# Kernel tuning notes

Measured on AMD Instinct MI355X. Metric: run time of the kernel, lower is better.

## Reference

```python
import jax, jax.numpy as jnp
import numpy as np

B, DIM, OC, H, W, HEADS = 4, 128, 128, 128, 128, 8
L = H * W
_BN_INV = 1.0 / (1.0 + 1e-5) ** 0.5  # eval-mode BN: running_mean=0, running_var=1


def conv2d(x, w, b=None, groups=1, pad=0):
    y = jax.lax.conv_general_dilated(
        x, w, (1, 1), [(pad, pad), (pad, pad)],
        dimension_numbers=('NCHW', 'OIHW', 'NCHW'),
        feature_group_count=groups)
    if b is not None:
        y = y + b[None, :, None, None]
    return y


def bn(x, g, b):
    return x * (g * _BN_INV)[None, :, None, None] + b[None, :, None, None]


def ln(x, g, b, eps=1e-5):
    m = jnp.mean(x, -1, keepdims=True)
    v = jnp.mean((x - m) ** 2, -1, keepdims=True)
    return (x - m) * jax.lax.rsqrt(v + eps) * g + b


def rope_tables(h, w, c, base=10000.0):
    k_max = c // 4
    theta = 1.0 / base ** (np.arange(k_max, dtype=np.float32) / k_max)
    gi, gj = np.meshgrid(np.arange(h, dtype=np.float32),
                         np.arange(w, dtype=np.float32), indexing='ij')
    ang = np.concatenate([gi[..., None] * theta, gj[..., None] * theta], -1)  # (h,w,c//2)
    return jnp.asarray(np.cos(ang)), jnp.asarray(np.sin(ang))


def apply_rope(x, cs, sn):  # x: (b,h,w,c); consecutive pairs = (re, im)
    xr, xi = x[..., 0::2], x[..., 1::2]
    return jnp.stack([cs * xr - sn * xi, sn * xr + cs * xi], -1).reshape(x.shape)


def linear_attn(x, qk_w, qk_b, lepe_w, lepe_b, h, w):
    b, n, c = x.shape
    hd = c // HEADS
    qk = x @ qk_w.T + qk_b
    q = jax.nn.elu(qk[..., :c]) + 1.0
    k = jax.nn.elu(qk[..., c:]) + 1.0
    cs, sn = rope_tables(h, w, c)

    def heads(t):  # (b,n,c) -> (b,HEADS,n,hd)
        return t.reshape(b, n, HEADS, hd).transpose(0, 2, 1, 3)

    q_r = heads(apply_rope(q.reshape(b, h, w, c), cs, sn).reshape(b, n, c))
    k_r = heads(apply_rope(k.reshape(b, h, w, c), cs, sn).reshape(b, n, c))
    qh, kh, vh = heads(q), heads(k), heads(x)
    k_mean = jnp.mean(kh, axis=2, keepdims=True)                      # (b,Hd,1,hd)
    z = 1.0 / (jnp.einsum('bhnd,bhmd->bhnm', qh, k_mean) + 1e-6)      # (b,Hd,n,1)
    s = n ** -0.5
    kv = jnp.einsum('bhnd,bhne->bhde', k_r * s, vh * s)               # (b,Hd,hd,hd)
    out = jnp.einsum('bhnd,bhde->bhne', q_r, kv) * z
    out = out.transpose(0, 2, 1, 3).reshape(b, n, c)
    v_img = x.reshape(b, h, w, c).transpose(0, 3, 1, 2)
    lepe = conv2d(v_img, lepe_w, lepe_b, groups=c, pad=1)
    return out + lepe.transpose(0, 2, 3, 1).reshape(b, n, c)


def fmt_block(xb, fw1, fb1, f_g, f_be, fw2, fb2, n_g, n_be):
    t = jnp.fft.fft2(xb)                                              # (B,C,H,W) complex
    wgt = jax.nn.relu(bn(conv2d(t.real, fw1, fb1), f_g, f_be))
    wgt = jax.nn.sigmoid(conv2d(wgt, fw2, fb2))
    f = jnp.abs(jnp.fft.ifft2(wgt * t))
    f = jax.nn.relu(bn(f, n_g, n_be))
    return f.reshape(f.shape[0], f.shape[1], -1).transpose(0, 2, 1)   # (B,L,C)


def _forward(x, c1_w, c1_b, c1_g, c1_be, cpe1_w, cpe1_b,
             fw1, fb1, f_g, f_be, fw2, fb2, nbn_g, nbn_be,
             ln1_g, ln1_b, d3w1, d3b1, d3w2, d5w1, d5b1, d5w2,
             ap_w, ap_b, ip2_w, ip2_b, dwc2_w, dwc2_b,
             qk_w, qk_b, lepe_w, lepe_b, op_w, op_b,
             cpe2_w, cpe2_b, ln2_g, ln2_b,
             ffn_w1, ffn_b1, ffn_w2, ffn_b2, po_w,
             red_w, red_b, red_g, red_be):
    Bb, C, Hh, Ww = x.shape
    Ll = Hh * Ww
    to_img = lambda t: t.reshape(Bb, Hh, Ww, C).transpose(0, 3, 1, 2)   # (B,L,C)->(B,C,H,W)
    to_seq = lambda t: t.transpose(0, 2, 3, 1).reshape(Bb, Ll, -1)       # (B,C,H,W)->(B,L,C)

    x_0 = jax.nn.relu(bn(conv2d(x, c1_w, c1_b), c1_g, c1_be))           # (B,OC,H,W)
    xt = to_seq(x + conv2d(x, cpe1_w, cpe1_b, groups=C, pad=1))
    shortcut = xt
    fmt1 = fmt_block(to_img(xt), fw1, fb1, f_g, f_be, fw2, fb2, nbn_g, nbn_be)

    x_s = ln(xt, ln1_g, ln1_b)
    xs_img = to_img(x_s)
    x_s3 = conv2d(conv2d(xs_img, d3w1, d3b1), d3w2, None, groups=C // 2, pad=1)
    x_s5 = conv2d(conv2d(xs_img, d5w1, d5b1), d5w2, None, groups=C // 2, pad=2)
    act_res = jax.nn.silu(to_seq(conv2d(xs_img, ap_w, ap_b)))

    def branch(t):  # (B,C/2,H,W) -> (B,L,C/2)
        t = conv2d(t, ip2_w, ip2_b)
        t = jax.nn.silu(conv2d(t, dwc2_w, dwc2_b, groups=C // 2, pad=1))
        return to_seq(t)

    a3 = linear_attn(branch(x_s3), qk_w, qk_b, lepe_w, lepe_b, Hh, Ww)
    a5 = linear_attn(branch(x_s5), qk_w, qk_b, lepe_w, lepe_b, Hh, Ww)
    xs = jnp.concatenate([a3, a5], -1)
    xs = to_seq(conv2d(to_img(xs * act_res), op_w, op_b))

    xt = shortcut + xs + fmt1
    xt = xt + to_seq(conv2d(to_img(xt), cpe2_w, cpe2_b, groups=C, pad=1))
    fmt2 = fmt_block(to_img(xt), fw1, fb1, f_g, f_be, fw2, fb2, nbn_g, nbn_be)
    h2 = ln(xt, ln2_g, ln2_b)
    ffn = jax.nn.gelu(h2 @ ffn_w1.T + ffn_b1, approximate=False) @ ffn_w2.T + ffn_b2
    xt = xt + ffn + fmt2

    xo = conv2d(to_img(xt), po_w)                                        # (B,OC,H,W)
    cat = jnp.concatenate([x_0, xo], 1)
    return jax.nn.relu(bn(conv2d(cat, red_w, red_b), red_g, red_be)) + x_0


def setup_inputs():
    key = jax.random.key(0)
    it = iter(jax.random.split(key, 64))

    def w(shape, s=0.05):
        return jax.random.normal(next(it), shape, jnp.float32) * s

    d, oc = DIM, OC
    ones = lambda n: jnp.ones((n,), jnp.float32)
    zeros = lambda n: jnp.zeros((n,), jnp.float32)
    return {
        'x': jax.random.normal(next(it), (B, d, H, W), jnp.float32),
        'c1_w': w((oc, d, 1, 1)), 'c1_b': w((oc,), 0.01), 'c1_g': ones(oc), 'c1_be': zeros(oc),
        'cpe1_w': w((d, 1, 3, 3)), 'cpe1_b': w((d,), 0.01),
        'fw1': w((d // 16, d, 1, 1)), 'fb1': w((d // 16,), 0.01),
        'f_g': ones(d // 16), 'f_be': zeros(d // 16),
        'fw2': w((d, d // 16, 1, 1)), 'fb2': w((d,), 0.01),
        'nbn_g': ones(d), 'nbn_be': zeros(d),
        'ln1_g': ones(d), 'ln1_b': zeros(d),
        'd3w1': w((d, d, 1, 1)), 'd3b1': w((d,), 0.01), 'd3w2': w((d // 2, 2, 3, 3)),
        'd5w1': w((d, d, 1, 1)), 'd5b1': w((d,), 0.01), 'd5w2': w((d // 2, 2, 5, 5)),
        'ap_w': w((d, d, 1, 1)), 'ap_b': w((d,), 0.01),
        'ip2_w': w((d // 2, d // 2, 1, 1)), 'ip2_b': w((d // 2,), 0.01),
        'dwc2_w': w((d // 2, 1, 3, 3)), 'dwc2_b': w((d // 2,), 0.01),
        'qk_w': w((d, d // 2)), 'qk_b': w((d,), 0.01),
        'lepe_w': w((d // 2, 1, 3, 3)), 'lepe_b': w((d // 2,), 0.01),
        'op_w': w((d, d, 1, 1)), 'op_b': w((d,), 0.01),
        'cpe2_w': w((d, 1, 3, 3)), 'cpe2_b': w((d,), 0.01),
        'ln2_g': ones(d), 'ln2_b': zeros(d),
        'ffn_w1': w((4, d)), 'ffn_b1': w((4,), 0.01),
        'ffn_w2': w((d, 4)), 'ffn_b2': w((d,), 0.01),
        'po_w': w((oc, d, 1, 1)),
        'red_w': w((oc, 2 * oc, 1, 1)), 'red_b': w((oc,), 0.01),
        'red_g': ones(oc), 'red_be': zeros(oc),
    }


def reference(x, c1_w, c1_b, c1_g, c1_be, cpe1_w, cpe1_b,
              fw1, fb1, f_g, f_be, fw2, fb2, nbn_g, nbn_be,
              ln1_g, ln1_b, d3w1, d3b1, d3w2, d5w1, d5b1, d5w2,
              ap_w, ap_b, ip2_w, ip2_b, dwc2_w, dwc2_b,
              qk_w, qk_b, lepe_w, lepe_b, op_w, op_b,
              cpe2_w, cpe2_b, ln2_g, ln2_b,
              ffn_w1, ffn_b1, ffn_w2, ffn_b2, po_w,
              red_w, red_b, red_g, red_be):
    return _forward(x, c1_w, c1_b, c1_g, c1_be, cpe1_w, cpe1_b,
                    fw1, fb1, f_g, f_be, fw2, fb2, nbn_g, nbn_be,
                    ln1_g, ln1_b, d3w1, d3b1, d3w2, d5w1, d5b1, d5w2,
                    ap_w, ap_b, ip2_w, ip2_b, dwc2_w, dwc2_b,
                    qk_w, qk_b, lepe_w, lepe_b, op_w, op_b,
                    cpe2_w, cpe2_b, ln2_g, ln2_b,
                    ffn_w1, ffn_b1, ffn_w2, ffn_b2, po_w,
                    red_w, red_b, red_g, red_be)
```

## Files before the change

kernel.cpp:

```cpp
#include <hip/hip_runtime.h>
#include <math.h>

typedef unsigned short bf16_t;
typedef __attribute__((ext_vector_type(8))) short short8;
typedef __attribute__((ext_vector_type(4))) float f32x4;

#define B_ 4
#define C_ 128
#define H_ 128
#define W_ 128
#define L_ (H_*W_)
#define NS  ((size_t)B_*L_*C_)
#define NH  ((size_t)B_*L_*64)
#define NSP ((size_t)L_*C_)
#define PI_F 3.14159265358979323846f
#define BN_INV 0.9999950000374997f
#define THETA_SC 0.8304820237218406f
#define TOTW 157148
#define W16SHIFT 107548
#define WOFF_PO 107612
#define WOFF_RED 123996

#define W2_ 66
#define L2_ (128*W2_)

__device__ __forceinline__ float ldf(bf16_t v){ return __uint_as_float(((unsigned)v)<<16); }
__device__ __forceinline__ bf16_t f2b(float f){
  unsigned u = __float_as_uint(f);
  u += 0x7fffu + ((u>>16)&1u);
  return (bf16_t)(u>>16);
}

#define WGSLOT ((size_t)B_*8*L_)
#define ACCSZ 2304
#define CWSZ 157184
#define CW16SZF 78592
#define WSF (6*NS + 3*NH + WGSLOT + ACCSZ + CWSZ + CW16SZF + 16)
__device__ float g_ws[WSF];

__global__ void k_probe(const bf16_t* __restrict__ xb, int* __restrict__ flag){
  __shared__ int vote;
  if (threadIdx.x == 0) vote = 0;
  __syncthreads();
  int bad = 0;
  for (int i = threadIdx.x; i < 2048; i += 256) {
    float v = ldf(xb[2*i]);
    if (!(fabsf(v) < 1e6f)) bad = 1;
  }
  if (bad) atomicOr(&vote, 1);
  __syncthreads();
  if (threadIdx.x == 0) *flag = vote;
}

struct P47 { const void* p[47]; };
__device__ __constant__ int c_wsz[47] = {
  16384,128,128,128,1152,128,1024,8,8,8,1024,128,128,128,128,128,
  16384,128,1152,16384,128,3200,16384,128,4096,64,576,64,8192,128,
  576,64,16384,128,1152,128,128,128,512,4,512,128,16384,32768,128,128,128};

__global__ __launch_bounds__(256) void k_cvt(P47 ps, const int* __restrict__ flagp,
                                             float* __restrict__ dst){
  int g = blockIdx.x*256 + threadIdx.x;
  if (g >= TOTW) return;
  int fl = *flagp;
  int idx = 0, off = g;
  while (off >= c_wsz[idx]) { off -= c_wsz[idx]; idx++; }
  const void* s = ps.p[idx];
  dst[g] = fl ? ((const float*)s)[off] : ldf(((const bf16_t*)s)[off]);
}

__global__ __launch_bounds__(256) void k_cvt16(const float* __restrict__ src, bf16_t* __restrict__ dst){
  int g = blockIdx.x*256 + threadIdx.x;
  if (g >= TOTW) return;
  dst[g + (g >= W16SHIFT ? 4 : 0)] = f2b(src[g]);
}

__global__ __launch_bounds__(256) void k_fuse_red(const float* __restrict__ po,
    const float* __restrict__ rw, bf16_t* __restrict__ dst16){
  int g = blockIdx.x*256 + threadIdx.x;
  int o = g >> 7, in = g & 127;
  float acc = 0.f;
  for (int j = 0; j < 128; j++) acc += rw[o*256 + 128 + j] * po[j*128 + in];
  dst16[o*256 + 128 + in] = f2b(acc);
}

__global__ void k_zero(float* p, int n){
  int i = blockIdx.x*256 + threadIdx.x;
  if (i < n) p[i] = 0.f;
}

__device__ __forceinline__ void tw_fwd(int lane, float* tc, float* ts) {
  sincosf(-PI_F * (float)lane * (1.f/64.f), &ts[0], &tc[0]);
  int i = 1;
  #pragma unroll
  for (int m = 32; m >= 1; m >>= 1, i++) {
    int k = lane & (m-1);
    sincosf(-PI_F * (float)k / (float)m, &ts[i], &tc[i]);
  }
}
__device__ __forceinline__ void tw_inv(int lane, float* tc, float* ts) {
  int i = 0;
  #pragma unroll
  for (int m = 1; m <= 32; m <<= 1, i++) {
    int k = lane & (m-1);
    sincosf(PI_F * (float)k / (float)m, &ts[i], &tc[i]);
  }
  sincosf(PI_F * (float)lane * (1.f/64.f), &ts[6], &tc[6]);
}

__device__ __forceinline__ void fft128_fwd(float& lor, float& loi, float& hir, float& hii,
                                           int lane, const float* tc, const float* ts) {
  {
    float s = ts[0], c = tc[0];
    float ar = lor, ai = loi;
    float dr = ar - hir, di = ai - hii;
    lor = ar + hir; loi = ai + hii;
    hir = dr*c - di*s; hii = dr*s + di*c;
  }
  int i = 1;
  #pragma unroll
  for (int m = 32; m >= 1; m >>= 1, i++) {
    float s = ts[i], c = tc[i];
    bool up = (lane & m) != 0;
    {
      float orr = __shfl_xor(lor, m), oii = __shfl_xor(loi, m);
      float sr = lor + orr, si = loi + oii;
      float dr = orr - lor, di = oii - loi;
      float tr = dr*c - di*s, ti = dr*s + di*c;
      lor = up ? tr : sr; loi = up ? ti : si;
    }
    {
      float orr = __shfl_xor(hir, m), oii = __shfl_xor(hii, m);
      float sr = hir + orr, si = hii + oii;
      float dr = orr - hir, di = oii - hii;
      float tr = dr*c - di*s, ti = dr*s + di*c;
      hir = up ? tr : sr; hii = up ? ti : si;
    }
  }
}

__device__ __forceinline__ void fft128_inv(float& lor, float& loi, float& hir, float& hii,
                                           int lane, const float* tc, const float* ts) {
  int i = 0;
  #pragma unroll
  for (int m = 1; m <= 32; m <<= 1, i++) {
    float s = ts[i], c = tc[i];
    bool up = (lane & m) != 0;
    {
      float orr = __shfl_xor(lor, m), oii = __shfl_xor(loi, m);
      float qr = orr*c - oii*s, qi = orr*s + oii*c;
      float lo_r = lor + qr, lo_i = loi + qi;
      float mr = lor*c - loi*s, mi = lor*s + loi*c;
      float up_r = orr - mr, up_i = oii - mi;
      lor = up ? up_r : lo_r; loi = up ? up_i : lo_i;
    }
    {
      float orr = __shfl_xor(hir, m), oii = __shfl_xor(hii, m);
      float qr = orr*c - oii*s, qi = orr*s + oii*c;
      float lo_r = hir + qr, lo_i = hii + qi;
      float mr = hir*c - hii*s, mi = hir*s + hii*c;
      float up_r = orr - mr, up_i = oii - mi;
      hir = up ? up_r : lo_r; hii = up ? up_i : lo_i;
    }
  }
  {
    float s = ts[6], c = tc[6];
    float qr = hir*c - hii*s, qi = hir*s + hii*c;
    float pr = lor, pi = loi;
    lor = pr + qr; loi = pi + qi;
    hir = pr - qr; hii = pi - qi;
  }
}

__global__ __launch_bounds__(256) void k_fft_row_fwd_half(
    const float* __restrict__ in, float* __restrict__ re, float* __restrict__ im) {
  __shared__ float T[64*130];
  int tid = threadIdx.x;
  int bid = blockIdx.x;
  int ch = (bid & 1) * 64;
  int h  = (bid >> 1) & 127;
  int b  = bid >> 8;
  const float* ip = in + ((size_t)b*L_ + (size_t)h*128)*128 + ch;
  #pragma unroll
  for (int it = 0; it < 8; it++) {
    int idx = it*256 + tid;
    int c4 = (idx & 15)*4, w = idx >> 4;
    float4 v = *(const float4*)(ip + (size_t)w*128 + c4);
    T[(c4+0)*130 + w] = v.x;
    T[(c4+1)*130 + w] = v.y;
    T[(c4+2)*130 + w] = v.z;
    T[(c4+3)*130 + w] = v.w;
  }
  __syncthreads();
  int lane = tid & 63, wv = tid >> 6;
  int rb = (int)(__brev((unsigned)lane) >> 26);
  int pe = (64 - lane) & 63;
  int po = 63 - lane;
  float tc[7], ts[7];
  tw_fwd(lane, tc, ts);
  #pragma unroll
  for (int t = 0; t < 8; t++) {
    int ca = wv*16 + 2*t, cb = ca + 1;
    float lor = T[ca*130 + lane],      loi = T[cb*130 + lane];
    float hir = T[ca*130 + 64 + lane], hii = T[cb*130 + 64 + lane];
    fft128_fwd(lor, loi, hir, hii, lane, tc, ts);
    float er  = __shfl(lor, rb), ei  = __shfl(loi, rb);
    float our = __shfl(hir, rb), oui = __shfl(hii, rb);
    float per = __shfl(er, pe),  pei = __shfl(ei, pe);
    float por = __shfl(our, po), poi = __shfl(oui, po);
    float ae_r = 0.5f*(er + per),  ae_i = 0.5f*(ei - pei);
    float be_r = 0.5f*(ei + pei),  be_i = 0.5f*(per - er);
    float ao_r = 0.5f*(our + por), ao_i = 0.5f*(oui - poi);
    float bo_r = 0.5f*(oui + poi), bo_i = 0.5f*(por - our);
    if (lane == 32) { ao_r = 0.f; ao_i = 0.f; bo_r = 0.f; bo_i = 0.f; }
    if (lane <= 32) {
      size_t ba = (size_t)(b*128 + ch + ca)*L2_ + (size_t)h*W2_ + 2*lane;
      size_t bb = (size_t)(b*128 + ch + cb)*L2_ + (size_t)h*W2_ + 2*lane;
      *(float2*)(re + ba) = make_float2(ae_r, ao_r);
      *(float2*)(im + ba) = make_float2(ae_i, ao_i);
      *(float2*)(re + bb) = make_float2(be_r, bo_r);
      *(float2*)(im + bb) = make_float2(be_i, bo_i);
    }
  }
}

__global__ __launch_bounds__(256) void k_fft_col_fwd_h(float* __restrict__ re, float* __restrict__ im) {
  __shared__ float Lre[128][34];
  __shared__ float Lim[128][34];
  int tid = threadIdx.x;
  size_t img = blockIdx.x >> 1;
  int w0 = (blockIdx.x & 1) * 33;
  float* rp = re + img * (size_t)L2_ + w0;
  float* ip = im + img * (size_t)L2_ + w0;
  for (int i = tid; i < 4224; i += 256) {
    int h = i / 33, wl = i - h*33;
    Lre[h][wl] = rp[(size_t)h*W2_ + wl];
    Lim[h][wl] = ip[(size_t)h*W2_ + wl];
  }
  __syncthreads();
  int lane = tid & 63, wv = tid >> 6;
  float tc[7], ts[7];
  tw_fwd(lane, tc, ts);
  for (int col = wv; col < 33; col += 4) {
    float lor = Lre[lane][col], loi = Lim[lane][col];
    float hir = Lre[lane+64][col], hii = Lim[lane+64][col];
    fft128_fwd(lor, loi, hir, hii, lane, tc, ts);
    Lre[lane][col]=lor; Lim[lane][col]=loi;
    Lre[lane+64][col]=hir; Lim[lane+64][col]=hii;
  }
  __syncthreads();
  for (int i = tid; i < 4224; i += 256) {
    int h = i / 33, wl = i - h*33;
    rp[(size_t)h*W2_ + wl] = Lre[h][wl];
    ip[(size_t)h*W2_ + wl] = Lim[h][wl];
  }
}

__global__ __launch_bounds__(256) void k_fft_col_inv_scaled_h(
    float* __restrict__ re, float* __restrict__ im,
    const float* __restrict__ wg1, const float* __restrict__ fw2,
    const float* __restrict__ fb2) {
  __shared__ float Lre[128][34];
  __shared__ float Lim[128][34];
  __shared__ float w2r[8];
  int tid = threadIdx.x;
  size_t img = blockIdx.x >> 1;
  int c = (int)(img & 127);
  int b = (int)(img >> 7);
  int w0 = (blockIdx.x & 1) * 33;
  if (tid < 8) w2r[tid] = fw2[c*8 + tid];
  float b2 = fb2[c];
  float* rp = re + img * (size_t)L2_ + w0;
  float* ip = im + img * (size_t)L2_ + w0;
  const float* wgp = wg1 + (size_t)b*8*L2_ + w0;
  __syncthreads();
  for (int i = tid; i < 4224; i += 256) {
    int h = i / 33, wl = i - h*33;
    size_t p = (size_t)h*W2_ + wl;
    float a = b2;
    #pragma unroll
    for (int o = 0; o < 8; o++) a += w2r[o] * wgp[(size_t)o*L2_ + p];
    float wgt = 1.f/(1.f+expf(-a));
    Lre[h][wl] = rp[p] * wgt;
    Lim[h][wl] = ip[p] * wgt;
  }
  __syncthreads();
  int lane = tid & 63, wv = tid >> 6;
  float tc[7], ts[7];
  tw_inv(lane, tc, ts);
  for (int col = wv; col < 33; col += 4) {
    float lor = Lre[lane][col], loi = Lim[lane][col];
    float hir = Lre[lane+64][col], hii = Lim[lane+64][col];
    fft128_inv(lor, loi, hir, hii, lane, tc, ts);
    Lre[lane][col]=lor*(1.f/128.f); Lim[lane][col]=loi*(1.f/128.f);
    Lre[lane+64][col]=hir*(1.f/128.f); Lim[lane+64][col]=hii*(1.f/128.f);
  }
  __syncthreads();
  for (int i = tid; i < 4224; i += 256) {
    int h = i / 33, wl = i - h*33;
    rp[(size_t)h*W2_ + wl] = Lre[h][wl];
    ip[(size_t)h*W2_ + wl] = Lim[h][wl];
  }
}

__global__ __launch_bounds__(256) void k_fft_row_inv_abs_seq_h(
    const float* __restrict__ re, const float* __restrict__ im,
    const float* __restrict__ ng, const float* __restrict__ nbe,
    const float* __restrict__ add1, const float* __restrict__ add2,
    float* __restrict__ out) {
  __shared__ float S[64*132];
  int tid = threadIdx.x;
  int bid = blockIdx.x;
  int ch = (bid & 1) * 64;
  int h  = (bid >> 1) & 127;
  int b  = bid >> 8;
  {
    const float* rbase = re + (size_t)(b*128 + ch)*L2_ + (size_t)h*W2_;
    const float* ibase = im + (size_t)(b*128 + ch)*L2_ + (size_t)h*W2_;
    for (int i = tid; i < 64*66; i += 256) {
      int c = i / 66, v = i - c*66;
      S[c*132 + v]      = rbase[(size_t)c*L2_ + v];
      S[c*132 + 66 + v] = ibase[(size_t)c*L2_ + v];
    }
  }
  __syncthreads();
  int lane = tid & 63, wv = tid >> 6;
  int rb = (int)(__brev((unsigned)lane) >> 26);
  int vlo = 2*rb, vhi = vlo + 1;
  float tc[7], ts[7];
  tw_inv(lane, tc, ts);
  float rr[8][4];
  #pragma unroll
  for (int t = 0; t < 8; t++) {
    int ca = wv*16 + 2*t, cb = ca + 1;
    const float* Sa = S + ca*132;
    const float* Sb = S + cb*132;
    float lor, loi, hir, hii;
    if (vlo <= 64) {
      float ar = Sa[vlo], ai = Sa[66+vlo], br = Sb[vlo], bi = Sb[66+vlo];
      lor = ar - bi; loi = ai + br;
    } else {
      int u = 128 - vlo;
      float ar = Sa[u], ai = Sa[66+u], br = Sb[u], bi = Sb[66+u];
      lor = ar + bi; loi = br - ai;
    }
    if (vhi <= 64) {
      float ar = Sa[vhi], ai = Sa[66+vhi], br = Sb[vhi], bi = Sb[66+vhi];
      hir = ar - bi; hii = ai + br;
    } else {
      int u = 128 - vhi;
      float ar = Sa[u], ai = Sa[66+u], br = Sb[u], bi = Sb[66+u];
      hir = ar + bi; hii = br - ai;
    }
    fft128_inv(lor, loi, hir, hii, lane, tc, ts);
    rr[t][0] = fabsf(lor);
    rr[t][1] = fabsf(loi);
    rr[t][2] = fabsf(hir);
    rr[t][3] = fabsf(hii);
  }
  __syncthreads();
  float* T = S;
  #pragma unroll
  for (int t = 0; t < 8; t++) {
    int ca = wv*16 + 2*t, cb = ca + 1;
    float sga = ng[ch+ca]*BN_INV, sba = nbe[ch+ca];
    float sgb = ng[ch+cb]*BN_INV, sbb = nbe[ch+cb];
    T[ca*130 + lane]      = fmaxf(rr[t][0]*(1.f/128.f)*sga + sba, 0.f);
    T[cb*130 + lane]      = fmaxf(rr[t][1]*(1.f/128.f)*sgb + sbb, 0.f);
    T[ca*130 + 64 + lane] = fmaxf(rr[t][2]*(1.f/128.f)*sga + sba, 0.f);
    T[cb*130 + 64 + lane] = fmaxf(rr[t][3]*(1.f/128.f)*sgb + sbb, 0.f);
  }
  __syncthreads();
  size_t sb0 = ((size_t)b*L_ + (size_t)h*128)*128 + ch;
  #pragma unroll
  for (int it = 0; it < 8; it++) {
    int idx = it*256 + tid;
    int c4 = (idx & 15)*4, w = idx >> 4;
    size_t off = sb0 + (size_t)w*128 + c4;
    float4 v;
    v.x = T[(c4+0)*130 + w];
    v.y = T[(c4+1)*130 + w];
    v.z = T[(c4+2)*130 + w];
    v.w = T[(c4+3)*130 + w];
    float4 x1 = *(const float4*)(add1 + off);
    float4 x2 = *(const float4*)(add2 + off);
    v.x += x1.x + x2.x; v.y += x1.y + x2.y;
    v.z += x1.z + x2.z; v.w += x1.w + x2.w;
    *(float4*)(out + off) = v;
  }
}

__global__ __launch_bounds__(256) void k_freq1_h(const float* __restrict__ tre,
    const float* __restrict__ fw1, const float* __restrict__ fb1,
    const float* __restrict__ fg, const float* __restrict__ fbe,
    float* __restrict__ wg1) {
  __shared__ float w1s[1024];
  int tid = threadIdx.x;
  for (int i = tid; i < 1024; i += 256) w1s[i] = fw1[i];
  __syncthreads();
  size_t g = (size_t)blockIdx.x*256 + tid;
  int p = (int)(g % L2_);
  int b = (int)(g / L2_);
  const float* tp = tre + (size_t)b*128*L2_ + p;
  float acc[8];
  #pragma unroll
  for (int o = 0; o < 8; o++) acc[o] = 0.f;
  for (int c = 0; c < 128; c++) {
    float v = tp[(size_t)c*L2_];
    #pragma unroll
    for (int o = 0; o < 8; o++) acc[o] += w1s[o*128+c]*v;
  }
  size_t ob = (size_t)b*8*L2_ + p;
  #pragma unroll
  for (int o = 0; o < 8; o++) {
    float v = (acc[o] + fb1[o]) * (fg[o]*BN_INV) + fbe[o];
    wg1[ob + (size_t)o*L2_] = fmaxf(v, 0.f);
  }
}

template<bool DUAL>
__global__ void k_p2s(const void* __restrict__ src, float* __restrict__ dst,
                      const float* __restrict__ add1, const float* __restrict__ add2,
                      const int* __restrict__ flagp) {
  __shared__ float tile[32][33];
  int fl = DUAL ? *flagp : 1;
  int b = blockIdx.z;
  int p0 = blockIdx.x*32, c0 = blockIdx.y*32;
  int tx = threadIdx.x, ty = threadIdx.y;
  size_t base_in = (size_t)b*NSP;
  #pragma unroll
  for (int k = 0; k < 4; k++) {
    size_t off = base_in + (size_t)(c0+ty+8*k)*L_ + p0 + tx;
    float v;
    if (DUAL && !fl) v = ldf(((const bf16_t*)src)[off]);
    else             v = ((const float*)src)[off];
    tile[ty+8*k][tx] = v;
  }
  __syncthreads();
  size_t base = (size_t)b*NSP;
  #pragma unroll
  for (int k = 0; k < 4; k++) {
    size_t idx = base + (size_t)(p0+ty+8*k)*C_ + c0 + tx;
    float v = tile[tx][ty+8*k];
    if (add1) v += add1[idx];
    if (add2) v += add2[idx];
    dst[idx] = v;
  }
}

template<int CC, int MODE>
__global__ __launch_bounds__(256) void k_dw3(const float* __restrict__ in,
    const float* __restrict__ w, const float* __restrict__ bias,
    float* __restrict__ out) {
  __shared__ float wl[9*CC];
  int tid = threadIdx.x;
  for (int i = tid; i < 9*CC; i += 256) {
    int tap = i / CC, ch = i % CC;
    wl[i] = w[ch*9 + tap];
  }
  __syncthreads();
  size_t g = (size_t)blockIdx.x*256 + tid;
  int c = (int)(g & (CC-1));
  float wr[9];
  #pragma unroll
  for (int t = 0; t < 9; t++) wr[t] = wl[t*CC + c];
  size_t s = g / CC;
  int w0 = (int)(s & 31) * 4;
  int hp = (int)((s >> 5) & 127);
  int b  = (int)(s >> 12);
  const float* ip = in + (size_t)b*L_*CC + c;
  float bi = bias[c];
  float a0 = bi, a1 = bi, a2 = bi, a3 = bi;
  #pragma unroll
  for (int dh = -1; dh <= 1; dh++) {
    int h2 = hp + dh;
    if ((unsigned)h2 >= 128u) continue;
    const float* rp = ip + (size_t)h2*W_*CC;
    float px[6];
    #pragma unroll
    for (int x = 0; x < 6; x++) {
      int w2 = w0 - 1 + x;
      px[x] = ((unsigned)w2 < 128u) ? rp[(size_t)w2*CC] : 0.f;
    }
    #pragma unroll
    for (int dw = 0; dw < 3; dw++) {
      float f = wr[(dh+1)*3 + dw];
      a0 += f*px[dw];   a1 += f*px[dw+1];
      a2 += f*px[dw+2]; a3 += f*px[dw+3];
    }
  }
  size_t tb = (size_t)b*L_ + (size_t)hp*W_ + w0;
  if (MODE == 0) {
    out[(tb+0)*CC + c] = in[(tb+0)*CC + c] + a0;
    out[(tb+1)*CC + c] = in[(tb+1)*CC + c] + a1;
    out[(tb+2)*CC + c] = in[(tb+2)*CC + c] + a2;
    out[(tb+3)*CC + c] = in[(tb+3)*CC + c] + a3;
  } else {
    out[(tb+0)*CC + c] = a0 / (1.f + expf(-a0));
    out[(tb+1)*CC + c] = a1 / (1.f + expf(-a1));
    out[(tb+2)*CC + c] = a2 / (1.f + expf(-a2));
    out[(tb+3)*CC + c] = a3 / (1.f + expf(-a3));
  }
}

template<int K>
__global__ __launch_bounds__(256) void k_gconv(const float* __restrict__ in,
    const float* __restrict__ w, float* __restrict__ out) {
  __shared__ float wl[K*K*128];
  int tid = threadIdx.x;
  for (int i = tid; i < 128*K*K; i += 256) {
    int tap = i >> 7, ch = i & 127;
    wl[i] = w[ch*(K*K) + tap];
  }
  __syncthreads();
  size_t g = (size_t)blockIdx.x*256 + tid;
  int oc = (int)(g & 63);
  float wx[K*K], wy[K*K];
  #pragma unroll
  for (int t = 0; t < K*K; t++) {
    wx[t] = wl[t*128 + 2*oc];
    wy[t] = wl[t*128 + 2*oc + 1];
  }
  size_t s = g >> 6;
  int w0 = (int)(s & 31) * 4;
  int hp = (int)((s >> 5) & 127);
  int b  = (int)(s >> 12);
  const float* ip = in + (size_t)b*L_*128 + 2*oc;
  constexpr int P = K/2;
  float a0 = 0.f, a1 = 0.f, a2 = 0.f, a3 = 0.f;
  #pragma unroll
  for (int kh = 0; kh < K; kh++) {
    int h2 = hp + kh - P;
    if ((unsigned)h2 >= 128u) continue;
    const float* rp = ip + (size_t)h2*W_*128;
    float2 px[K+3];
    #pragma unroll
    for (int x = 0; x < K+3; x++) {
      int w2 = w0 - P + x;
      px[x] = ((unsigned)w2 < 128u) ? *(const float2*)(rp + (size_t)w2*128)
                                    : make_float2(0.f, 0.f);
    }
    #pragma unroll
    for (int kw = 0; kw < K; kw++) {
      float fx = wx[kh*K + kw], fy = wy[kh*K + kw];
      a0 += fx*px[kw+0].x + fy*px[kw+0].y;
      a1 += fx*px[kw+1].x + fy*px[kw+1].y;
      a2 += fx*px[kw+2].x + fy*px[kw+2].y;
      a3 += fx*px[kw+3].x + fy*px[kw+3].y;
    }
  }
  size_t tb = (size_t)b*L_ + (size_t)hp*W_ + w0;
  out[(tb+0)*64 + oc] = a0;
  out[(tb+1)*64 + oc] = a1;
  out[(tb+2)*64 + oc] = a2;
  out[(tb+3)*64 + oc] = a3;
}

template<int CIN, int COUT, int EPI, bool MUL>
__global__ __launch_bounds__(256) void k_mfma_tok(
    const float* __restrict__ in, const float* __restrict__ mulp,
    const bf16_t* __restrict__ W16, const float* __restrict__ bias,
    float* __restrict__ out) {
  constexpr int NO = COUT/16;
  constexpr int KS = (CIN >= 128) ? 4 : (CIN/32);
  int tid = threadIdx.x;
  int lane = tid & 63, wv = tid >> 6;
  int m = lane & 15, q = lane >> 4;
  size_t t0 = (size_t)blockIdx.x*64 + (size_t)wv*16;
  f32x4 acc[NO];
  #pragma unroll
  for (int i = 0; i < NO; i++) acc[i] = (f32x4){0.f,0.f,0.f,0.f};
  for (int kc = 0; kc < CIN; kc += KS*32) {
    float4 A[KS][2];
    #pragma unroll
    for (int kk = 0; kk < KS; kk++) {
      const float* ap = in + (t0 + m)*CIN + kc + kk*32 + q*8;
      A[kk][0] = *(const float4*)ap;
      A[kk][1] = *(const float4*)(ap + 4);
    }
    if (MUL) {
      #pragma unroll
      for (int kk = 0; kk < KS; kk++) {
        const float* mp = mulp + (t0 + m)*CIN + kc + kk*32 + q*8;
        float4 m0 = *(const float4*)mp;
        float4 m1 = *(const float4*)(mp + 4);
        A[kk][0].x*=m0.x; A[kk][0].y*=m0.y; A[kk][0].z*=m0.z; A[kk][0].w*=m0.w;
        A[kk][1].x*=m1.x; A[kk][1].y*=m1.y; A[kk][1].z*=m1.z; A[kk][1].w*=m1.w;
      }
    }
    #pragma unroll
    for (int kk = 0; kk < KS; kk++) {
      union { short s[8]; short8 v; } af;
      af.s[0]=(short)f2b(A[kk][0].x); af.s[1]=(short)f2b(A[kk][0].y);
      af.s[2]=(short)f2b(A[kk][0].z); af.s[3]=(short)f2b(A[kk][0].w);
      af.s[4]=(short)f2b(A[kk][1].x); af.s[5]=(short)f2b(A[kk][1].y);
      af.s[6]=(short)f2b(A[kk][1].z); af.s[7]=(short)f2b(A[kk][1].w);
      #pragma unroll
      for (int o = 0; o < NO; o++) {
        short8 bf = *(const short8*)(W16 + (size_t)(o*16 + m)*CIN + kc + kk*32 + q*8);
        acc[o] = __builtin_amdgcn_mfma_f32_16x16x32_bf16(af.v, bf, acc[o], 0, 0, 0);
      }
    }
  }
  #pragma unroll
  for (int o = 0; o < NO; o++) {
    float bv = (EPI >= 1) ? bias[o*16 + m] : 0.f;
    #pragma unroll
    for (int r = 0; r < 4; r++) {
      int row = q*4 + r;
      float v = acc[o][r] + bv;
      if (EPI == 2) v = v / (1.f + expf(-v));
      if (EPI == 3) v = v > 0.f ? v + 1.f : expf(v);
      out[(t0 + row)*COUT + o*16 + m] = v;
    }
  }
}

__global__ __launch_bounds__(256) void k_mfma_c1(
    const float* __restrict__ in, const bf16_t* __restrict__ W16,
    const float* __restrict__ bias, const float* __restrict__ gam,
    const float* __restrict__ bet, float* __restrict__ out) {
  constexpr int NO = 8;
  int tid = threadIdx.x;
  int lane = tid & 63, wv = tid >> 6;
  int m = lane & 15, q = lane >> 4;
  size_t t0 = (size_t)blockIdx.x*64 + (size_t)wv*16;
  f32x4 acc[NO];
  #pragma unroll
  for (int i = 0; i < NO; i++) acc[i] = (f32x4){0.f,0.f,0.f,0.f};
  {
    float4 A[4][2];
    #pragma unroll
    for (int kk = 0; kk < 4; kk++) {
      const float* ap = in + (t0 + m)*128 + kk*32 + q*8;
      A[kk][0] = *(const float4*)ap;
      A[kk][1] = *(const float4*)(ap + 4);
    }
    #pragma unroll
    for (int kk = 0; kk < 4; kk++) {
      union { short s[8]; short8 v; } af;
      af.s[0]=(short)f2b(A[kk][0].x); af.s[1]=(short)f2b(A[kk][0].y);
      af.s[2]=(short)f2b(A[kk][0].z); af.s[3]=(short)f2b(A[kk][0].w);
      af.s[4]=(short)f2b(A[kk][1].x); af.s[5]=(short)f2b(A[kk][1].y);
      af.s[6]=(short)f2b(A[kk][1].z); af.s[7]=(short)f2b(A[kk][1].w);
      #pragma unroll
      for (int o = 0; o < NO; o++) {
        short8 bf = *(const short8*)(W16 + (size_t)(o*16 + m)*128 + kk*32 + q*8);
        acc[o] = __builtin_amdgcn_mfma_f32_16x16x32_bf16(af.v, bf, acc[o], 0, 0, 0);
      }
    }
  }
  #pragma unroll
  for (int o = 0; o < NO; o++) {
    int oc = o*16 + m;
    float bi = bias[oc], gm = gam[oc]*BN_INV, be = bet[oc];
    #pragma unroll
    for (int r = 0; r < 4; r++) {
      int row = q*4 + r;
      float v = acc[o][r] + bi;
      out[(t0 + row)*128 + oc] = fmaxf(v*gm + be, 0.f);
    }
  }
}

__global__ __launch_bounds__(256) void k_mfma_red(
    const float* __restrict__ x0s, const float* __restrict__ xt4,
    const bf16_t* __restrict__ W16, const float* __restrict__ bias,
    const float* __restrict__ gam, const float* __restrict__ bet,
    void* __restrict__ out, const int* __restrict__ flagp) {
  __shared__ float T[128*65];
  constexpr int NO = 8;
  int fl = *flagp;
  int tid = threadIdx.x;
  int lane = tid & 63, wv = tid >> 6;
  int m = lane & 15, q = lane >> 4;
  size_t t0 = (size_t)blockIdx.x*64;
  size_t tw = t0 + (size_t)wv*16;
  f32x4 acc[NO];
  #pragma unroll
  for (int i = 0; i < NO; i++) acc[i] = (f32x4){0.f,0.f,0.f,0.f};
  #pragma unroll
  for (int half = 0; half < 2; half++) {
    const float* src = half ? xt4 : x0s;
    float4 A[4][2];
    #pragma unroll
    for (int kk = 0; kk < 4; kk++) {
      const float* ap = src + (tw + m)*128 + kk*32 + q*8;
      A[kk][0] = *(const float4*)ap;
      A[kk][1] = *(const float4*)(ap + 4);
    }
    #pragma unroll
    for (int kk = 0; kk < 4; kk++) {
      union { short s[8]; short8 v; } af;
      af.s[0]=(short)f2b(A[kk][0].x); af.s[1]=(short)f2b(A[kk][0].y);
      af.s[2]=(short)f2b(A[kk][0].z); af.s[3]=(short)f2b(A[kk][0].w);
      af.s[4]=(short)f2b(A[kk][1].x); af.s[5]=(short)f2b(A[kk][1].y);
      af.s[6]=(short)f2b(A[kk][1].z); af.s[7]=(short)f2b(A[kk][1].w);
      #pragma unroll
      for (int o = 0; o < NO; o++) {
        short8 bf = *(const short8*)(W16 + (size_t)(o*16 + m)*256 + half*128 + kk*32 + q*8);
        acc[o] = __builtin_amdgcn_mfma_f32_16x16x32_bf16(af.v, bf, acc[o], 0, 0, 0);
      }
    }
  }
  #pragma unroll
  for (int ot = 0; ot < NO; ot++) {
    int o = ot*16 + m;
    float bi = bias[o], gm = gam[o]*BN_INV, be = bet[o];
    #pragma unroll
    for (int r = 0; r < 4; r++) {
      int row = q*4 + r;
      float v = acc[ot][r] + bi;
      v = fmaxf(v*gm + be, 0.f);
      v += x0s[(tw + row)*128 + o];
      T[o*65 + wv*16 + row] = v;
    }
  }
  __syncthreads();
  int b = (int)(t0 >> 14);
  int p0 = (int)(t0 & (L_-1));
  if (!fl) {
    bf16_t* op = (bf16_t*)out;
    for (int i = tid; i < 8192; i += 256) {
      int o = i >> 6, tk = i & 63;
      op[((size_t)b*128 + o)*L_ + p0 + tk] = f2b(T[o*65 + tk]);
    }
  } else {
    float* op = (float*)out;
    for (int i = tid; i < 8192; i += 256) {
      int o = i >> 6, tk = i & 63;
      op[((size_t)b*128 + o)*L_ + p0 + tk] = T[o*65 + tk];
    }
  }
}

__global__ __launch_bounds__(256) void k_ln(const float* __restrict__ in,
    const float* __restrict__ g, const float* __restrict__ be, float* __restrict__ out) {
  int tid = threadIdx.x, lane = tid & 63;
  size_t t = (size_t)blockIdx.x*4 + (tid >> 6);
  const float* row = in + t*128;
  float2 v = *(const float2*)(row + lane*2);
  float s = v.x + v.y, ss = v.x*v.x + v.y*v.y;
  #pragma unroll
  for (int m = 1; m < 64; m <<= 1) { s += __shfl_xor(s, m); ss += __shfl_xor(ss, m); }
  float mean = s*(1.f/128.f);
  float inv = rsqrtf(ss*(1.f/128.f) - mean*mean + 1e-5f);
  float2 o;
  o.x = (v.x-mean)*inv*g[lane*2]   + be[lane*2];
  o.y = (v.y-mean)*inv*g[lane*2+1] + be[lane*2+1];
  *(float2*)(out + t*128 + lane*2) = o;
}

__global__ __launch_bounds__(256) void k_ln_ffn(const float* __restrict__ in,
    const float* __restrict__ g, const float* __restrict__ be,
    const float* __restrict__ w1, const float* __restrict__ b1,
    const float* __restrict__ w2, const float* __restrict__ b2,
    float* __restrict__ out) {
  int tid = threadIdx.x, lane = tid & 63;
  size_t t = (size_t)blockIdx.x*4 + (tid >> 6);
  const float* row = in + t*128;
  float2 v = *(const float2*)(row + lane*2);
  float s = v.x + v.y, ss = v.x*v.x + v.y*v.y;
  #pragma unroll
  for (int m = 1; m < 64; m <<= 1) { s += __shfl_xor(s, m); ss += __shfl_xor(ss, m); }
  float mean = s*(1.f/128.f);
  float inv = rsqrtf(ss*(1.f/128.f) - mean*mean + 1e-5f);
  float hx = (v.x-mean)*inv*g[lane*2]   + be[lane*2];
  float hy = (v.y-mean)*inv*g[lane*2+1] + be[lane*2+1];
  float hp0 = hx*w1[0*128+lane*2] + hy*w1[0*128+lane*2+1];
  float hp1 = hx*w1[1*128+lane*2] + hy*w1[1*128+lane*2+1];
  float hp2 = hx*w1[2*128+lane*2] + hy*w1[2*128+lane*2+1];
  float hp3 = hx*w1[3*128+lane*2] + hy*w1[3*128+lane*2+1];
  #pragma unroll
  for (int m = 1; m < 64; m <<= 1) {
    hp0 += __shfl_xor(hp0, m); hp1 += __shfl_xor(hp1, m);
    hp2 += __shfl_xor(hp2, m); hp3 += __shfl_xor(hp3, m);
  }
  float hv0, hv1, hv2, hv3;
  { float a = hp0 + b1[0]; hv0 = 0.5f*a*(1.f+erff(a*0.7071067811865476f)); }
  { float a = hp1 + b1[1]; hv1 = 0.5f*a*(1.f+erff(a*0.7071067811865476f)); }
  { float a = hp2 + b1[2]; hv2 = 0.5f*a*(1.f+erff(a*0.7071067811865476f)); }
  { float a = hp3 + b1[3]; hv3 = 0.5f*a*(1.f+erff(a*0.7071067811865476f)); }
  int cx = lane*2, cy = lane*2+1;
  float2 o;
  o.x = hv0*w2[cx*4+0] + hv1*w2[cx*4+1] + hv2*w2[cx*4+2] + hv3*w2[cx*4+3] + b2[cx];
  o.y = hv0*w2[cy*4+0] + hv1*w2[cy*4+1] + hv2*w2[cy*4+2] + hv3*w2[cy*4+3] + b2[cy];
  *(float2*)(out + t*128 + lane*2) = o;
}

__global__ __launch_bounds__(256) void k_kv(
    const float* __restrict__ qk, const float* __restrict__ v,
    float* __restrict__ akv_g, float* __restrict__ aks_g) {
  __shared__ float kvred[512];
  __shared__ float ksred[64];
  int tid = threadIdx.x;
  for (int i = tid; i < 512; i += 256) kvred[i] = 0.f;
  if (tid < 64) ksred[tid] = 0.f;
  __syncthreads();
  int lane = tid & 63, wv = tid >> 6;
  size_t t0 = (size_t)blockIdx.x * 64;
  int b = (int)(t0 >> 14);
  int pr = lane >> 1;
  float theta = exp2f(-(float)(pr & 15) * THETA_SC);
  bool use_i = pr < 16;
  int hbase = lane & 56;
  float akv[8];
  #pragma unroll
  for (int d = 0; d < 8; d++) akv[d] = 0.f;
  float aks = 0.f;
  for (int it = 0; it < 16; it++) {
    size_t t = t0 + (size_t)wv*16 + it;
    float k = qk[t*128 + 64 + lane];
    float xv = v[t*64 + lane];
    int l = (int)(t & (L_-1));
    float pos = use_i ? (float)(l >> 7) : (float)(l & 127);
    float sn, cs; sincosf(pos*theta, &sn, &cs);
    float kp = __shfl_xor(k, 1);
    float kr = (lane & 1) ? (sn*kp + cs*k) : (cs*k - sn*kp);
    #pragma unroll
    for (int d = 0; d < 8; d++) {
      float krd = __shfl(kr, hbase + d);
      akv[d] += krd * xv;
    }
    aks += k;
  }
  int h8 = lane >> 3, e = lane & 7;
  #pragma unroll
  for (int d = 0; d < 8; d++)
    atomicAdd(&kvred[h8*64 + d*8 + e], akv[d]);
  atomicAdd(&ksred[lane], aks);
  __syncthreads();
  for (int i = tid; i < 512; i += 256) atomicAdd(&akv_g[b*512 + i], kvred[i]);
  if (tid < 64) atomicAdd(&aks_g[b*64 + tid], ksred[tid]);
}

__global__ __launch_bounds__(256) void k_attn2(
    const float* __restrict__ qk, const float* __restrict__ x,
    const float* __restrict__ akv_g, const float* __restrict__ aks_g,
    const float* __restrict__ lw, const float* __restrict__ lb,
    float* __restrict__ out, int coff) {
  __shared__ float kv[512];
  __shared__ float km[64];
  __shared__ float lwl[576];
  int tid = threadIdx.x;
  size_t t0 = (size_t)blockIdx.x * 32;
  int b = (int)(t0 >> 14);
  const float invn = 1.f/16384.f;
  for (int i = tid; i < 512; i += 256) kv[i] = akv_g[b*512 + i]*invn;
  if (tid < 64) km[tid] = aks_g[b*64 + tid]*invn;
  for (int i = tid; i < 576; i += 256) lwl[i] = lw[i];
  __syncthreads();
  int lane = tid & 63, wv = tid >> 6;
  int pr = lane >> 1;
  float theta = exp2f(-(float)(pr & 15) * THETA_SC);
  bool use_i = pr < 16;
  int hbase = lane & 56, e = lane & 7;
  float lbv = lb[lane];
  const float* xb = x + ((size_t)b << 14) * 64;
  for (int it = 0; it < 8; it++) {
    size_t t = t0 + (size_t)wv*8 + it;
    int l = (int)(t & (L_-1));
    int ipos = l >> 7, jpos = l & 127;
    float q = qk[t*128 + lane];
    float p = q * km[lane];
    p += __shfl_xor(p, 1); p += __shfl_xor(p, 2); p += __shfl_xor(p, 4);
    float z = 1.f/(p + 1e-6f);
    float pos = use_i ? (float)ipos : (float)jpos;
    float sn, cs; sincosf(pos*theta, &sn, &cs);
    float qp = __shfl_xor(q, 1);
    float qr = (lane & 1) ? (sn*qp + cs*q) : (cs*q - sn*qp);
    float acc = 0.f;
    #pragma unroll
    for (int d = 0; d < 8; d++) {
      float qrd = __shfl(qr, hbase + d);
      acc += qrd * kv[hbase*8 + d*8 + e];
    }
    acc *= z;
    float lp = lbv;
    #pragma unroll
    for (int dh = -1; dh <= 1; dh++) {
      int h2 = ipos + dh; if ((unsigned)h2 >= 128u) continue;
      #pragma unroll
      for (int dw = -1; dw <= 1; dw++) {
        int w2 = jpos + dw; if ((unsigned)w2 >= 128u) continue;
        lp += lwl[lane*9 + (dh+1)*3 + (dw+1)] * xb[((size_t)(h2 << 7) + w2)*64 + lane];
      }
    }
    out[t*128 + coff + lane] = acc + lp;
  }
}

extern "C" void kernel_launch(void* const* d_in, const int* in_sizes, int n_in,
                              void* d_out, int out_size, void* d_ws, size_t ws_size,
                              hipStream_t stream) {
  (void)in_sizes; (void)n_in; (void)out_size;

  float* base;
  if (ws_size >= WSF * sizeof(float)) {
    base = (float*)d_ws;
  } else {
    void* p = nullptr;
    hipGetSymbolAddress(&p, HIP_SYMBOL(g_ws));
    base = (float*)p;
  }
  float* P0 = base;
  float* PA = base + 1*NS;
  float* PB = base + 2*NS;
  float* PC = base + 3*NS;
  float* PD = base + 4*NS;
  float* PF = base + 5*NS;
  float* H0 = base + 6*NS;
  float* H1 = H0 + NH;
  float* H2 = H1 + NH;
  float* WG = H2 + NH;
  float* ACC = WG + WGSLOT;
  float* CW  = ACC + ACCSZ;
  bf16_t* CW16 = (bf16_t*)(CW + CWSZ);
  int*   FLG = (int*)(CW + CWSZ + CW16SZF);

  static const int wsz[47] = {
    16384,128,128,128,1152,128,1024,8,8,8,1024,128,128,128,128,128,
    16384,128,1152,16384,128,3200,16384,128,4096,64,576,64,8192,128,
    576,64,16384,128,1152,128,128,128,512,4,512,128,16384,32768,128,128,128};
  int woff[47]; { int a = 0; for (int i = 0; i < 47; i++){ woff[i] = a; a += wsz[i]; } }
  const float* Wf[47]; for (int i = 0; i < 47; i++) Wf[i] = CW + woff[i];
  auto W16 = [&](int i){ return (const bf16_t*)(CW16 + woff[i] + (woff[i] >= W16SHIFT ? 4 : 0)); };
  const float *c1_b=Wf[1], *c1_g=Wf[2], *c1_be=Wf[3], *cpe1_w=Wf[4],
    *cpe1_b=Wf[5], *fw1=Wf[6], *fb1=Wf[7], *f_g=Wf[8], *f_be=Wf[9], *fw2=Wf[10],
    *fb2=Wf[11], *nbn_g=Wf[12], *nbn_be=Wf[13], *ln1_g=Wf[14], *ln1_b=Wf[15],
    *d3b1=Wf[17], *d3w2=Wf[18], *d5b1=Wf[20],
    *d5w2=Wf[21], *ap_b=Wf[23], *ip2_b=Wf[25],
    *dwc2_w=Wf[26], *dwc2_b=Wf[27], *qk_b=Wf[29], *lepe_w=Wf[30],
    *lepe_b=Wf[31], *op_b=Wf[33], *cpe2_w=Wf[34], *cpe2_b=Wf[35],
    *ln2_g=Wf[36], *ln2_b=Wf[37], *ffn_w1=Wf[38], *ffn_b1=Wf[39], *ffn_w2=Wf[40],
    *ffn_b2=Wf[41], *red_b=Wf[44], *red_g=Wf[45], *red_be=Wf[46];
  const bf16_t *c1_w16=W16(0), *d3w1_16=W16(16), *d5w1_16=W16(19), *ap_w16=W16(22),
    *ip2_w16=W16(24), *qk_w16=W16(28), *op_w16=W16(32), *red_w16=W16(43);

  const void* x = d_in[0];

  k_probe<<<1, 256, 0, stream>>>((const bf16_t*)x, FLG);
  P47 ps; for (int i = 0; i < 47; i++) ps.p[i] = d_in[i+1];
  k_cvt<<<(TOTW+255)/256, 256, 0, stream>>>(ps, FLG, CW);
  k_cvt16<<<(TOTW+255)/256, 256, 0, stream>>>(CW, CW16);
  k_fuse_red<<<64, 256, 0, stream>>>(CW + WOFF_PO, CW + WOFF_RED,
                                     (bf16_t*)(CW16 + WOFF_RED + 4));

  dim3 tgrid(512, 4, 4), tblk(32, 8);

  auto fmt_fused = [&](const float* seq_in, float* re, float* im,
                       const float* add1, const float* add2, float* outp) {
    k_fft_row_fwd_half<<<1024, 256, 0, stream>>>(seq_in, re, im);
    k_fft_col_fwd_h<<<1024, 256, 0, stream>>>(re, im);
    k_freq1_h<<<132, 256, 0, stream>>>(re, fw1, fb1, f_g, f_be, WG);
    k_fft_col_inv_scaled_h<<<1024, 256, 0, stream>>>(re, im, WG, fw2, fb2);
    k_fft_row_inv_abs_seq_h<<<1024, 256, 0, stream>>>(re, im, nbn_g, nbn_be, add1, add2, outp);
  };

  auto attn = [&](const float* brin, float* qkbuf, int coff) {
    k_zero<<<9, 256, 0, stream>>>(ACC, 2304);
    k_mfma_tok<64,128,3,false><<<1024, 256, 0, stream>>>(brin, nullptr, qk_w16, qk_b, qkbuf);
    k_kv<<<1024, 256, 0, stream>>>(qkbuf, brin, ACC, ACC + B_*512);
    k_attn2<<<2048, 256, 0, stream>>>(qkbuf, brin, ACC, ACC + B_*512, lepe_w, lepe_b, PF, coff);
  };

  k_p2s<true><<<tgrid, tblk, 0, stream>>>(x, PA, nullptr, nullptr, FLG);
  k_mfma_c1<<<1024, 256, 0, stream>>>(PA, c1_w16, c1_b, c1_g, c1_be, P0);
  k_dw3<128,0><<<8192, 256, 0, stream>>>(PA, cpe1_w, cpe1_b, PB);
  k_ln<<<16384, 256, 0, stream>>>(PB, ln1_g, ln1_b, PA);
  k_mfma_tok<128,128,1,false><<<1024, 256, 0, stream>>>(PA, nullptr, d3w1_16, d3b1, PD);
  k_gconv<3><<<4096, 256, 0, stream>>>(PD, d3w2, H0);
  k_mfma_tok<128,128,1,false><<<1024, 256, 0, stream>>>(PA, nullptr, d5w1_16, d5b1, PD);
  k_gconv<5><<<4096, 256, 0, stream>>>(PD, d5w2, H1);
  k_mfma_tok<128,128,2,false><<<1024, 256, 0, stream>>>(PA, nullptr, ap_w16, ap_b, PA);
  k_mfma_tok<64,64,1,false><<<1024, 256, 0, stream>>>(H0, nullptr, ip2_w16, ip2_b, H2);
  k_dw3<64,1><<<4096, 256, 0, stream>>>(H2, dwc2_w, dwc2_b, H0);
  attn(H0, PD, 0);
  k_mfma_tok<64,64,1,false><<<1024, 256, 0, stream>>>(H1, nullptr, ip2_w16, ip2_b, H2);
  k_dw3<64,1><<<4096, 256, 0, stream>>>(H2, dwc2_w, dwc2_b, H1);
  attn(H1, PD, 64);
  k_mfma_tok<128,128,1,true><<<1024, 256, 0, stream>>>(PF, PA, op_w16, op_b, PF);
  fmt_fused(PB, PC, PD, PB, PF, PB);
  k_dw3<128,0><<<8192, 256, 0, stream>>>(PB, cpe2_w, cpe2_b, PC);
  k_ln_ffn<<<16384, 256, 0, stream>>>(PC, ln2_g, ln2_b, ffn_w1, ffn_b1, ffn_w2, ffn_b2, PF);
  fmt_fused(PC, PB, PD, PC, PF, PC);
  k_mfma_red<<<1024, 256, 0, stream>>>(P0, PC, red_w16, red_b, red_g, red_be, d_out, FLG);
}
```

Before: 965.6 us.

## Fuse LayerNorm with three 1x1 projections into one MFMA kernel

Replaces the separate LayerNorm kernel and three token-wise MFMA GEMMs (d3, d5, ap) with a single kernel. It normalizes each 16-token tile in registers, converts it to bf16, and issues all three GEMMs against the shared A fragments. This removes one full-tensor write and three reads of the normalized activations, plus three launches. In exchange it uses 24 accumulator tiles per wave, which raises register pressure and may lower occupancy. The d5 output moves to buffer PF so the d3 and d5 results can coexist.

```diff
diff --git a/kernel.cpp b/kernel.cpp
--- a/kernel.cpp
+++ b/kernel.cpp
@@ -616,6 +616,88 @@
   }
 }
 
+__global__ __launch_bounds__(256) void k_mfma_ln3(
+    const float* __restrict__ in,
+    const float* __restrict__ lng, const float* __restrict__ lnb,
+    const bf16_t* __restrict__ Wd3, const float* __restrict__ bd3,
+    const bf16_t* __restrict__ Wd5, const float* __restrict__ bd5,
+    const bf16_t* __restrict__ Wap, const float* __restrict__ bap,
+    float* __restrict__ outd3, float* __restrict__ outd5, float* __restrict__ outap) {
+  __shared__ float gs[128], bs[128];
+  int tid = threadIdx.x;
+  if (tid < 128) { gs[tid] = lng[tid]; bs[tid] = lnb[tid]; }
+  __syncthreads();
+  int lane = tid & 63, wv = tid >> 6;
+  int m = lane & 15, q = lane >> 4;
+  size_t t0 = (size_t)blockIdx.x*64 + (size_t)wv*16;
+  float4 A[4][2];
+  #pragma unroll
+  for (int kk = 0; kk < 4; kk++) {
+    const float* ap = in + (t0 + m)*128 + kk*32 + q*8;
+    A[kk][0] = *(const float4*)ap;
+    A[kk][1] = *(const float4*)(ap + 4);
+  }
+  float s = 0.f, ss = 0.f;
+  #pragma unroll
+  for (int kk = 0; kk < 4; kk++)
+    #pragma unroll
+    for (int h = 0; h < 2; h++) {
+      float4 v = A[kk][h];
+      s  += v.x + v.y + v.z + v.w;
+      ss += v.x*v.x + v.y*v.y + v.z*v.z + v.w*v.w;
+    }
+  s  += __shfl_xor(s, 16);  s  += __shfl_xor(s, 32);
+  ss += __shfl_xor(ss, 16); ss += __shfl_xor(ss, 32);
+  float mean = s*(1.f/128.f);
+  float inv = rsqrtf(ss*(1.f/128.f) - mean*mean + 1e-5f);
+  short8 af[4];
+  #pragma unroll
+  for (int kk = 0; kk < 4; kk++) {
+    union { short sh[8]; short8 v; } u;
+    #pragma unroll
+    for (int h = 0; h < 2; h++) {
+      const float* vp = (const float*)&A[kk][h];
+      #pragma unroll
+      for (int j = 0; j < 4; j++) {
+        int c = kk*32 + q*8 + h*4 + j;
+        float x = (vp[j] - mean)*inv*gs[c] + bs[c];
+        u.sh[h*4+j] = (short)f2b(x);
+      }
+    }
+    af[kk] = u.v;
+  }
+  f32x4 acc[24];
+  #pragma unroll
+  for (int i = 0; i < 24; i++) acc[i] = (f32x4){0.f,0.f,0.f,0.f};
+  #pragma unroll
+  for (int kk = 0; kk < 4; kk++) {
+    #pragma unroll
+    for (int o = 0; o < 8; o++) {
+      size_t woff = (size_t)(o*16 + m)*128 + kk*32 + q*8;
+      short8 b3 = *(const short8*)(Wd3 + woff);
+      acc[o]    = __builtin_amdgcn_mfma_f32_16x16x32_bf16(af[kk], b3, acc[o],    0, 0, 0);
+      short8 b5 = *(const short8*)(Wd5 + woff);
+      acc[8+o]  = __builtin_amdgcn_mfma_f32_16x16x32_bf16(af[kk], b5, acc[8+o],  0, 0, 0);
+      short8 ba = *(const short8*)(Wap + woff);
+      acc[16+o] = __builtin_amdgcn_mfma_f32_16x16x32_bf16(af[kk], ba, acc[16+o], 0, 0, 0);
+    }
+  }
+  #pragma unroll
+  for (int o = 0; o < 8; o++) {
+    int oc = o*16 + m;
+    float b3 = bd3[oc], b5 = bd5[oc], ba = bap[oc];
+    #pragma unroll
+    for (int r = 0; r < 4; r++) {
+      int row = q*4 + r;
+      size_t idx = (t0 + row)*128 + oc;
+      outd3[idx] = acc[o][r] + b3;
+      outd5[idx] = acc[8+o][r] + b5;
+      float v = acc[16+o][r] + ba;
+      outap[idx] = v / (1.f + expf(-v));
+    }
+  }
+}
+
 __global__ __launch_bounds__(256) void k_mfma_c1(
     const float* __restrict__ in, const bf16_t* __restrict__ W16,
     const float* __restrict__ bias, const float* __restrict__ gam,
@@ -732,23 +814,6 @@
       op[((size_t)b*128 + o)*L_ + p0 + tk] = T[o*65 + tk];
     }
   }
-}
-
-__global__ __launch_bounds__(256) void k_ln(const float* __restrict__ in,
-    const float* __restrict__ g, const float* __restrict__ be, float* __restrict__ out) {
-  int tid = threadIdx.x, lane = tid & 63;
-  size_t t = (size_t)blockIdx.x*4 + (tid >> 6);
-  const float* row = in + t*128;
-  float2 v = *(const float2*)(row + lane*2);
-  float s = v.x + v.y, ss = v.x*v.x + v.y*v.y;
-  #pragma unroll
-  for (int m = 1; m < 64; m <<= 1) { s += __shfl_xor(s, m); ss += __shfl_xor(ss, m); }
-  float mean = s*(1.f/128.f);
-  float inv = rsqrtf(ss*(1.f/128.f) - mean*mean + 1e-5f);
-  float2 o;
-  o.x = (v.x-mean)*inv*g[lane*2]   + be[lane*2];
-  o.y = (v.y-mean)*inv*g[lane*2+1] + be[lane*2+1];
-  *(float2*)(out + t*128 + lane*2) = o;
 }
 
 __global__ __launch_bounds__(256) void k_ln_ffn(const float* __restrict__ in,
@@ -967,12 +1032,10 @@
   k_p2s<true><<<tgrid, tblk, 0, stream>>>(x, PA, nullptr, nullptr, FLG);
   k_mfma_c1<<<1024, 256, 0, stream>>>(PA, c1_w16, c1_b, c1_g, c1_be, P0);
   k_dw3<128,0><<<8192, 256, 0, stream>>>(PA, cpe1_w, cpe1_b, PB);
-  k_ln<<<16384, 256, 0, stream>>>(PB, ln1_g, ln1_b, PA);
-  k_mfma_tok<128,128,1,false><<<1024, 256, 0, stream>>>(PA, nullptr, d3w1_16, d3b1, PD);
+  k_mfma_ln3<<<1024, 256, 0, stream>>>(PB, ln1_g, ln1_b,
+      d3w1_16, d3b1, d5w1_16, d5b1, ap_w16, ap_b, PD, PF, PA);
   k_gconv<3><<<4096, 256, 0, stream>>>(PD, d3w2, H0);
-  k_mfma_tok<128,128,1,false><<<1024, 256, 0, stream>>>(PA, nullptr, d5w1_16, d5b1, PD);
-  k_gconv<5><<<4096, 256, 0, stream>>>(PD, d5w2, H1);
-  k_mfma_tok<128,128,2,false><<<1024, 256, 0, stream>>>(PA, nullptr, ap_w16, ap_b, PA);
+  k_gconv<5><<<4096, 256, 0, stream>>>(PF, d5w2, H1);
   k_mfma_tok<64,64,1,false><<<1024, 256, 0, stream>>>(H0, nullptr, ip2_w16, ip2_b, H2);
   k_dw3<64,1><<<4096, 256, 0, stream>>>(H2, dwc2_w, dwc2_b, H0);
   attn(H0, PD, 0);
```

After: 933.3 us. -3.3%, faster.
